# Performance work log

Measured on AMD Instinct MI355X. Metric: run time of the kernel, lower is better.

## Reference

```python
import jax, jax.numpy as jnp
import numpy as np

# 2nd-order Sobel kernels (kornia get_sobel_kernel2d_2nd_order): d2/dx2, d2/dxdy, d2/dy2
_KXX = np.array([[1., -2., 1.], [2., -4., 2.], [1., -2., 1.]], np.float32)
_KXY = np.array([[-1., 0., 1.], [0., 0., 0.], [1., 0., -1.]], np.float32)
_KERNELS = jnp.asarray(np.stack([_KXX, _KXY, _KXX.T])[:, None])  # (3,1,3,3)


def setup_inputs() -> dict:
    key = jax.random.key(0)
    x = jax.random.normal(key, (16, 3, 1024, 1024), dtype=jnp.float32)
    return {"x": x}


def reference(x):
    scale = 1.0
    B, C, H, W = x.shape
    # spatial_gradient_2nd_order: replicate pad + 3x3 conv per channel
    xp = jnp.pad(x.reshape(B * C, 1, H, W), ((0, 0), (0, 0), (1, 1), (1, 1)), mode='edge')
    g = jax.lax.conv_general_dilated(xp, _KERNELS, (1, 1), 'VALID')  # (B*C, 3, H, W)
    gxx, gxy, gyy = g[:, 0], g[:, 1], g[:, 2]
    # abs determinant of Hessian, clamp
    scores = jnp.abs(gxx * gyy - gxy * gxy) * (scale ** 4)
    scores = jnp.maximum(scores, 1e-6).reshape(B, C, H, W)
    # NMS via 3x3 max-pool (stride 1, SAME): keep only local maxima
    pooled = jax.lax.reduce_window(scores, -jnp.inf, jax.lax.max,
                                   (1, 1, 3, 3), (1, 1, 1, 1), 'SAME')
    scores = jnp.where(scores == pooled, scores, jnp.zeros((), scores.dtype))
    # global max normalization (adaptive_max_pool2d to 1x1)
    smax = jnp.max(scores, axis=(2, 3), keepdims=True)  # (B,C,1,1)
    return scores / smax
```

## Files before the change

kernel.cpp:

```cpp
#include <hip/hip_runtime.h>

#define H 1024
#define W 1024
#define HW (H * W)
#define STRIP 16

__device__ __forceinline__ float score_ref(
    float a00, float a01, float a02,
    float a10, float a11, float a12,
    float a20, float a21, float a22)
{
#pragma clang fp contract(off)
    float gxx = fmaf(-2.0f, a01, a00);
    gxx = gxx + a02;
    gxx = fmaf(2.0f, a10, gxx);
    gxx = fmaf(-4.0f, a11, gxx);
    gxx = fmaf(2.0f, a12, gxx);
    gxx = gxx + a20;
    gxx = fmaf(-2.0f, a21, gxx);
    gxx = gxx + a22;
    float gxy = a02 - a00;
    gxy = gxy + a20;
    gxy = gxy - a22;
    float gyy = fmaf(2.0f, a01, a00);
    gyy = gyy + a02;
    gyy = fmaf(-2.0f, a10, gyy);
    gyy = fmaf(-4.0f, a11, gyy);
    gyy = fmaf(-2.0f, a12, gyy);
    gyy = gyy + a20;
    gyy = fmaf(2.0f, a21, gyy);
    gyy = gyy + a22;

    float p1 = gxx * gyy;
    float p2 = gxy * gxy;
    float det = p1 - p2;
    float s = fabsf(det);
    return s > 1e-6f ? s : 1e-6f;
}

struct Row8 { float a[8]; };

__device__ __forceinline__ Row8 load_row8(const float* __restrict__ prow, int c, int t)
{
    const float4 m = *(const float4*)(prow + c);
    int lc = c - 2; lc = lc < 0 ? 0 : lc;
    const float2 L = *(const float2*)(prow + lc);
    int rc = c + 4; rc = rc > (W - 2) ? (W - 2) : rc;
    const float2 R = *(const float2*)(prow + rc);
    float l0 = L.x, l1 = L.y;
    if (t == 0) l1 = L.x;
    float q0 = R.x, q1 = R.y;
    if (t == 255) q0 = R.y;
    Row8 r;
    r.a[0] = l0; r.a[1] = l1;
    r.a[2] = m.x; r.a[3] = m.y; r.a[4] = m.z; r.a[5] = m.w;
    r.a[6] = q0; r.a[7] = q1;
    return r;
}

__global__ __launch_bounds__(256) void hess_max_kernel(
    const float* __restrict__ x, unsigned int* __restrict__ pmax)
{
    const int plane = blockIdx.y;
    const int y0 = blockIdx.x * STRIP;
    const int t = threadIdx.x;
    const int c = t * 4;
    const float* px = x + (size_t)plane * HW;

    Row8 r0 = load_row8(px + (size_t)(y0 - 1 < 0 ? 0 : y0 - 1) * W, c, t);
    Row8 r1 = load_row8(px + (size_t)y0 * W, c, t);
    Row8 r2 = load_row8(px + (size_t)(y0 + 1 > H - 1 ? H - 1 : y0 + 1) * W, c, t);
    Row8 r3 = load_row8(px + (size_t)(y0 + 2 > H - 1 ? H - 1 : y0 + 2) * W, c, t);

    float smax = 1e-6f;
#pragma unroll
    for (int i = 0; i < STRIP; ++i) {
        const int sy = y0 + i;
        const int pf = sy + 3 > H - 1 ? H - 1 : sy + 3;
        Row8 r4 = load_row8(px + (size_t)pf * W, c, t);

        float P[6], Q[6], Rv[6];
#pragma unroll
        for (int k = 0; k < 6; ++k) {
            P[k] = fmaf(2.0f, r1.a[k + 1], r0.a[k + 1]) + r2.a[k + 1];
            Q[k] = fmaf(-2.0f, r1.a[k + 1], r0.a[k + 1]) + r2.a[k + 1];
            Rv[k] = r0.a[k + 1] - r2.a[k + 1];
        }
#pragma unroll
        for (int j = 0; j < 4; ++j) {
            float gxx = fmaf(-2.0f, P[j + 1], P[j]) + P[j + 2];
            float gyy = fmaf(2.0f, Q[j + 1], Q[j]) + Q[j + 2];
            float gxy = Rv[j + 2] - Rv[j];
            float det = fmaf(gxx, gyy, -(gxy * gxy));
            smax = fmaxf(smax, fabsf(det));
        }
        r0 = r1; r1 = r2; r2 = r3; r3 = r4;
    }

#pragma unroll
    for (int off = 32; off > 0; off >>= 1)
        smax = fmaxf(smax, __shfl_down(smax, off));
    if ((t & 63) == 0)
        atomicMax(pmax + plane, __float_as_uint(smax));
}

struct S6 { float s[6]; };

__device__ __forceinline__ S6 score_row_exact(const Row8& A, const Row8& B, const Row8& C)
{
    S6 o;
#pragma unroll
    for (int i = 0; i < 6; ++i)
        o.s[i] = score_ref(A.a[i], A.a[i + 1], A.a[i + 2],
                           B.a[i], B.a[i + 1], B.a[i + 2],
                           C.a[i], C.a[i + 1], C.a[i + 2]);
    return o;
}

__global__ __launch_bounds__(256) void hess_nms_kernel(
    const float* __restrict__ x, const unsigned int* __restrict__ pmax,
    float* __restrict__ out)
{
    const int plane = blockIdx.y;
    const int y0 = blockIdx.x * STRIP;
    const int t = threadIdx.x;
    const int c = t * 4;
    const float* px = x + (size_t)plane * HW;
    float* po = out + (size_t)plane * HW;
    const float inv = 1.0f / __uint_as_float(pmax[plane]);

    Row8 rm2 = load_row8(px + (size_t)(y0 - 2 < 0 ? 0 : y0 - 2) * W, c, t);
    Row8 r0  = load_row8(px + (size_t)(y0 - 1 < 0 ? 0 : y0 - 1) * W, c, t);
    Row8 r1  = load_row8(px + (size_t)y0 * W, c, t);
    Row8 r2  = load_row8(px + (size_t)(y0 + 1 > H - 1 ? H - 1 : y0 + 1) * W, c, t);
    Row8 r3  = load_row8(px + (size_t)(y0 + 2 > H - 1 ? H - 1 : y0 + 2) * W, c, t);

    S6 zero;
#pragma unroll
    for (int i = 0; i < 6; ++i) zero.s[i] = 0.0f;

    S6 sp = zero;
    if (y0 > 0) sp = score_row_exact(rm2, r0, r1);
    S6 sc_ = score_row_exact(r0, r1, r2);

#pragma unroll
    for (int i = 0; i < STRIP; ++i) {
        const int sy = y0 + i;
        const int pf = sy + 3 > H - 1 ? H - 1 : sy + 3;
        Row8 r4 = load_row8(px + (size_t)pf * W, c, t);

        S6 sn = zero;
        if (sy + 1 < H) sn = score_row_exact(r1, r2, r3);

        float4 o;
        float* ov = (float*)&o;
#pragma unroll
        for (int j = 0; j < 4; ++j) {
            float s = sc_.s[j + 1];
            float m = fmaxf(fmaxf(fmaxf(sp.s[j], sp.s[j + 1]), fmaxf(sp.s[j + 2], sc_.s[j])),
                            fmaxf(fmaxf(sc_.s[j + 1], sc_.s[j + 2]),
                                  fmaxf(fmaxf(sn.s[j], sn.s[j + 1]), sn.s[j + 2])));
            ov[j] = (s == m) ? s * inv : 0.0f;
        }
        *(float4*)(po + (size_t)sy * W + c) = o;

        r0 = r1; r1 = r2; r2 = r3; r3 = r4;
        sp = sc_; sc_ = sn;
    }
}

extern "C" void kernel_launch(void* const* d_in, const int* in_sizes, int n_in,
                              void* d_out, int out_size, void* d_ws, size_t ws_size,
                              hipStream_t stream) {
    const float* x = (const float*)d_in[0];
    float* out = (float*)d_out;
    unsigned int* pmax = (unsigned int*)d_ws;
    const int planes = in_sizes[0] / HW;

    hipMemsetAsync(pmax, 0, planes * sizeof(unsigned int), stream);

    dim3 grid(H / STRIP, planes);
    hess_max_kernel<<<grid, 256, 0, stream>>>(x, pmax);
    hess_nms_kernel<<<grid, 256, 0, stream>>>(x, pmax, out);
}
```

Before: 425.3 us.

## Stage input rows through an LDS ring buffer and double strip height

Each thread now issues one float4 global load per row and writes it into a 6-slot LDS ring with replicated edge padding. Neighbour windows are then read back from LDS as two float4s, replacing the overlapping halo float2 global loads. STRIP grows from 16 to 32 so less vertical halo is reloaded per strip. The cost is a __syncthreads per row, LDS traffic, and loops that are no longer unrolled, which may limit memory-level parallelism.

New measurement: 414.6 us. 1.03x faster.

```diff
diff --git a/kernel.cpp b/kernel.cpp
--- a/kernel.cpp
+++ b/kernel.cpp
@@ -3,7 +3,9 @@
 #define H 1024
 #define W 1024
 #define HW (H * W)
-#define STRIP 16
+#define STRIP 32
+#define LDSROW 1032
+#define NSLOT 6
 
 __device__ __forceinline__ float score_ref(
     float a00, float a01, float a02,
@@ -40,51 +42,66 @@
 
 struct Row8 { float a[8]; };
 
-__device__ __forceinline__ Row8 load_row8(const float* __restrict__ prow, int c, int t)
-{
-    const float4 m = *(const float4*)(prow + c);
-    int lc = c - 2; lc = lc < 0 ? 0 : lc;
-    const float2 L = *(const float2*)(prow + lc);
-    int rc = c + 4; rc = rc > (W - 2) ? (W - 2) : rc;
-    const float2 R = *(const float2*)(prow + rc);
-    float l0 = L.x, l1 = L.y;
-    if (t == 0) l1 = L.x;
-    float q0 = R.x, q1 = R.y;
-    if (t == 255) q0 = R.y;
+__device__ __forceinline__ float4 load_row4(const float* __restrict__ px, int row, int t)
+{
+    row = row < 0 ? 0 : (row > H - 1 ? H - 1 : row);
+    return *(const float4*)(px + (size_t)row * W + (t << 2));
+}
+
+__device__ __forceinline__ void stage_row(float* lds, int slot, float4 v, int t)
+{
+    float* p = lds + slot * LDSROW;
+    float* q = p + 2 + (t << 2);
+    *(float2*)(q)     = make_float2(v.x, v.y);
+    *(float2*)(q + 2) = make_float2(v.z, v.w);
+    if (t == 0)   { p[0] = v.x; p[1] = v.x; }
+    if (t == 255) { p[1026] = v.w; p[1027] = v.w; }
+}
+
+__device__ __forceinline__ Row8 read_win(const float* lds, int slot, int t)
+{
+    const float* p = lds + slot * LDSROW + (t << 2);
+    float4 lo = *(const float4*)(p);
+    float4 hi = *(const float4*)(p + 4);
     Row8 r;
-    r.a[0] = l0; r.a[1] = l1;
-    r.a[2] = m.x; r.a[3] = m.y; r.a[4] = m.z; r.a[5] = m.w;
-    r.a[6] = q0; r.a[7] = q1;
+    r.a[0] = lo.x; r.a[1] = lo.y; r.a[2] = lo.z; r.a[3] = lo.w;
+    r.a[4] = hi.x; r.a[5] = hi.y; r.a[6] = hi.z; r.a[7] = hi.w;
     return r;
 }
 
 __global__ __launch_bounds__(256) void hess_max_kernel(
     const float* __restrict__ x, unsigned int* __restrict__ pmax)
 {
+    __shared__ float lds[NSLOT * LDSROW];
     const int plane = blockIdx.y;
     const int y0 = blockIdx.x * STRIP;
     const int t = threadIdx.x;
-    const int c = t * 4;
     const float* px = x + (size_t)plane * HW;
 
-    Row8 r0 = load_row8(px + (size_t)(y0 - 1 < 0 ? 0 : y0 - 1) * W, c, t);
-    Row8 r1 = load_row8(px + (size_t)y0 * W, c, t);
-    Row8 r2 = load_row8(px + (size_t)(y0 + 1 > H - 1 ? H - 1 : y0 + 1) * W, c, t);
-    Row8 r3 = load_row8(px + (size_t)(y0 + 2 > H - 1 ? H - 1 : y0 + 2) * W, c, t);
+    stage_row(lds, 0, load_row4(px, y0 - 1, t), t);
+    stage_row(lds, 1, load_row4(px, y0, t), t);
+    float4 gv = load_row4(px, y0 + 1, t);
+    __syncthreads();
+    Row8 A = read_win(lds, 0, t);
+    Row8 B = read_win(lds, 1, t);
 
     float smax = 1e-6f;
-#pragma unroll
+    int sw = 2;
     for (int i = 0; i < STRIP; ++i) {
         const int sy = y0 + i;
-        const int pf = sy + 3 > H - 1 ? H - 1 : sy + 3;
-        Row8 r4 = load_row8(px + (size_t)pf * W, c, t);
+        stage_row(lds, sw, gv, t);
+        __syncthreads();
+        gv = load_row4(px, sy + 2, t);
+
+        Row8 C = read_win(lds, sw, t);
+        sw = (sw + 1 == NSLOT) ? 0 : sw + 1;
 
         float P[6], Q[6], Rv[6];
 #pragma unroll
         for (int k = 0; k < 6; ++k) {
-            P[k] = fmaf(2.0f, r1.a[k + 1], r0.a[k + 1]) + r2.a[k + 1];
-            Q[k] = fmaf(-2.0f, r1.a[k + 1], r0.a[k + 1]) + r2.a[k + 1];
-            Rv[k] = r0.a[k + 1] - r2.a[k + 1];
+            P[k]  = fmaf(2.0f, B.a[k + 1], A.a[k + 1]) + C.a[k + 1];
+            Q[k]  = fmaf(-2.0f, B.a[k + 1], A.a[k + 1]) + C.a[k + 1];
+            Rv[k] = A.a[k + 1] - C.a[k + 1];
         }
 #pragma unroll
         for (int j = 0; j < 4; ++j) {
@@ -94,7 +111,7 @@
             float det = fmaf(gxx, gyy, -(gxy * gxy));
             smax = fmaxf(smax, fabsf(det));
         }
-        r0 = r1; r1 = r2; r2 = r3; r3 = r4;
+        A = B; B = C;
     }
 
 #pragma unroll
@@ -121,19 +138,26 @@
     const float* __restrict__ x, const unsigned int* __restrict__ pmax,
     float* __restrict__ out)
 {
+    __shared__ float lds[NSLOT * LDSROW];
     const int plane = blockIdx.y;
     const int y0 = blockIdx.x * STRIP;
     const int t = threadIdx.x;
-    const int c = t * 4;
     const float* px = x + (size_t)plane * HW;
     float* po = out + (size_t)plane * HW;
     const float inv = 1.0f / __uint_as_float(pmax[plane]);
 
-    Row8 rm2 = load_row8(px + (size_t)(y0 - 2 < 0 ? 0 : y0 - 2) * W, c, t);
-    Row8 r0  = load_row8(px + (size_t)(y0 - 1 < 0 ? 0 : y0 - 1) * W, c, t);
-    Row8 r1  = load_row8(px + (size_t)y0 * W, c, t);
-    Row8 r2  = load_row8(px + (size_t)(y0 + 1 > H - 1 ? H - 1 : y0 + 1) * W, c, t);
-    Row8 r3  = load_row8(px + (size_t)(y0 + 2 > H - 1 ? H - 1 : y0 + 2) * W, c, t);
+    stage_row(lds, 0, load_row4(px, y0 - 2, t), t);
+    stage_row(lds, 1, load_row4(px, y0 - 1, t), t);
+    stage_row(lds, 2, load_row4(px, y0,     t), t);
+    stage_row(lds, 3, load_row4(px, y0 + 1, t), t);
+    stage_row(lds, 4, load_row4(px, y0 + 2, t), t);
+    float4 gv = load_row4(px, y0 + 3, t);
+    __syncthreads();
+    Row8 rm2 = read_win(lds, 0, t);
+    Row8 r0  = read_win(lds, 1, t);
+    Row8 r1  = read_win(lds, 2, t);
+    Row8 r2  = read_win(lds, 3, t);
+    Row8 r3  = read_win(lds, 4, t);
 
     S6 zero;
 #pragma unroll
@@ -143,11 +167,12 @@
     if (y0 > 0) sp = score_row_exact(rm2, r0, r1);
     S6 sc_ = score_row_exact(r0, r1, r2);
 
-#pragma unroll
+    int sw = 5;
     for (int i = 0; i < STRIP; ++i) {
         const int sy = y0 + i;
-        const int pf = sy + 3 > H - 1 ? H - 1 : sy + 3;
-        Row8 r4 = load_row8(px + (size_t)pf * W, c, t);
+        stage_row(lds, sw, gv, t);
+        __syncthreads();
+        gv = load_row4(px, sy + 4, t);
 
         S6 sn = zero;
         if (sy + 1 < H) sn = score_row_exact(r1, r2, r3);
@@ -162,9 +187,11 @@
                                   fmaxf(fmaxf(sn.s[j], sn.s[j + 1]), sn.s[j + 2])));
             ov[j] = (s == m) ? s * inv : 0.0f;
         }
-        *(float4*)(po + (size_t)sy * W + c) = o;
-
-        r0 = r1; r1 = r2; r2 = r3; r3 = r4;
+        *(float4*)(po + (size_t)sy * W + (t << 2)) = o;
+
+        Row8 r4 = read_win(lds, sw, t);
+        sw = (sw + 1 == NSLOT) ? 0 : sw + 1;
+        r1 = r2; r2 = r3; r3 = r4;
         sp = sc_; sc_ = sn;
     }
 }
```

## Stage input rows through an LDS ring via async global_load_lds and double strip height

Applied to the files above, without the earlier changes.

Both kernels now stream input rows into a six-slot LDS ring using the direct global-to-LDS load builtin, with vmcnt waits plus barriers pipelining the prefetch, instead of each thread issuing three overlapping global loads per row. The strip height doubles to 32 rows, which cuts the redundant halo-row reads between blocks, and the output uses nontemporal stores. This removes duplicated global traffic for the neighbour columns and gives explicit prefetch depth. In exchange it adds per-row block barriers, LDS use that can lower occupancy, and fragile hand-counted waitcnt logic.

Result: faster. 411.7 us (-3.2%).

```diff
diff --git a/kernel.cpp b/kernel.cpp
--- a/kernel.cpp
+++ b/kernel.cpp
@@ -3,7 +3,30 @@
 #define H 1024
 #define W 1024
 #define HW (H * W)
-#define STRIP 16
+#define STRIP 32
+#define SLOTF 1024
+#define RING 6
+
+typedef __attribute__((address_space(3))) float lds_f;
+typedef const __attribute__((address_space(1))) float g_f;
+typedef float nfloat4 __attribute__((ext_vector_type(4)));
+
+__device__ __forceinline__ void gload16(const float* g, float* l) {
+    __builtin_amdgcn_global_load_lds((g_f*)g, (lds_f*)l, 16, 0, 0);
+}
+
+template<int N>
+__device__ __forceinline__ void wait_vm_barrier() {
+    asm volatile("s_waitcnt vmcnt(%0)\n\ts_barrier" :: "i"(N) : "memory");
+}
+__device__ __forceinline__ void barrier_only() {
+    asm volatile("s_barrier" ::: "memory");
+}
+
+__device__ __forceinline__ void stage(const float* px, int row, float* slotbase, int wq, int t) {
+    row = row < 0 ? 0 : (row > H - 1 ? H - 1 : row);
+    gload16(px + (size_t)row * W + (t << 2), slotbase + wq);
+}
 
 __device__ __forceinline__ float score_ref(
     float a00, float a01, float a02,
@@ -40,51 +63,57 @@
 
 struct Row8 { float a[8]; };
 
-__device__ __forceinline__ Row8 load_row8(const float* __restrict__ prow, int c, int t)
-{
-    const float4 m = *(const float4*)(prow + c);
-    int lc = c - 2; lc = lc < 0 ? 0 : lc;
-    const float2 L = *(const float2*)(prow + lc);
-    int rc = c + 4; rc = rc > (W - 2) ? (W - 2) : rc;
-    const float2 R = *(const float2*)(prow + rc);
-    float l0 = L.x, l1 = L.y;
-    if (t == 0) l1 = L.x;
-    float q0 = R.x, q1 = R.y;
-    if (t == 255) q0 = R.y;
+__device__ __forceinline__ Row8 read_win(const float* p, int t)
+{
+    const int c = t << 2;
+    const float2 L  = *(const float2*)(p + (t == 0 ? 0 : c - 2));
+    const float4 M  = *(const float4*)(p + c);
+    const float2 Rr = *(const float2*)(p + (t == 255 ? 1022 : c + 4));
     Row8 r;
-    r.a[0] = l0; r.a[1] = l1;
-    r.a[2] = m.x; r.a[3] = m.y; r.a[4] = m.z; r.a[5] = m.w;
-    r.a[6] = q0; r.a[7] = q1;
+    r.a[0] = L.x;
+    r.a[1] = (t == 0) ? L.x : L.y;
+    r.a[2] = M.x; r.a[3] = M.y; r.a[4] = M.z; r.a[5] = M.w;
+    r.a[6] = (t == 255) ? Rr.y : Rr.x;
+    r.a[7] = Rr.y;
     return r;
 }
 
 __global__ __launch_bounds__(256) void hess_max_kernel(
     const float* __restrict__ x, unsigned int* __restrict__ pmax)
 {
+    __shared__ float lds[RING * SLOTF];
     const int plane = blockIdx.y;
     const int y0 = blockIdx.x * STRIP;
     const int t = threadIdx.x;
-    const int c = t * 4;
+    const int wq = (t >> 6) << 8;
     const float* px = x + (size_t)plane * HW;
 
-    Row8 r0 = load_row8(px + (size_t)(y0 - 1 < 0 ? 0 : y0 - 1) * W, c, t);
-    Row8 r1 = load_row8(px + (size_t)y0 * W, c, t);
-    Row8 r2 = load_row8(px + (size_t)(y0 + 1 > H - 1 ? H - 1 : y0 + 1) * W, c, t);
-    Row8 r3 = load_row8(px + (size_t)(y0 + 2 > H - 1 ? H - 1 : y0 + 2) * W, c, t);
+#pragma unroll
+    for (int k = 0; k < RING; ++k)
+        stage(px, y0 - 1 + k, lds + k * SLOTF, wq, t);
+    wait_vm_barrier<4>();
+    Row8 A = read_win(lds, t);
+    Row8 B = read_win(lds + SLOTF, t);
 
     float smax = 1e-6f;
-#pragma unroll
+    int si = 0, sr = 2;
     for (int i = 0; i < STRIP; ++i) {
-        const int sy = y0 + i;
-        const int pf = sy + 3 > H - 1 ? H - 1 : sy + 3;
-        Row8 r4 = load_row8(px + (size_t)pf * W, c, t);
+        if (i < STRIP - 4) {
+            stage(px, y0 + i + 5, lds + si * SLOTF, wq, t);
+            si = si + 1 == RING ? 0 : si + 1;
+            wait_vm_barrier<4>();
+        } else {
+            wait_vm_barrier<0>();
+        }
+        Row8 C = read_win(lds + sr * SLOTF, t);
+        sr = sr + 1 == RING ? 0 : sr + 1;
 
         float P[6], Q[6], Rv[6];
 #pragma unroll
         for (int k = 0; k < 6; ++k) {
-            P[k] = fmaf(2.0f, r1.a[k + 1], r0.a[k + 1]) + r2.a[k + 1];
-            Q[k] = fmaf(-2.0f, r1.a[k + 1], r0.a[k + 1]) + r2.a[k + 1];
-            Rv[k] = r0.a[k + 1] - r2.a[k + 1];
+            P[k]  = fmaf(2.0f, B.a[k + 1], A.a[k + 1]) + C.a[k + 1];
+            Q[k]  = fmaf(-2.0f, B.a[k + 1], A.a[k + 1]) + C.a[k + 1];
+            Rv[k] = A.a[k + 1] - C.a[k + 1];
         }
 #pragma unroll
         for (int j = 0; j < 4; ++j) {
@@ -94,7 +123,7 @@
             float det = fmaf(gxx, gyy, -(gxy * gxy));
             smax = fmaxf(smax, fabsf(det));
         }
-        r0 = r1; r1 = r2; r2 = r3; r3 = r4;
+        A = B; B = C;
     }
 
 #pragma unroll
@@ -121,19 +150,24 @@
     const float* __restrict__ x, const unsigned int* __restrict__ pmax,
     float* __restrict__ out)
 {
+    __shared__ float lds[RING * SLOTF];
     const int plane = blockIdx.y;
     const int y0 = blockIdx.x * STRIP;
     const int t = threadIdx.x;
-    const int c = t * 4;
+    const int wq = (t >> 6) << 8;
     const float* px = x + (size_t)plane * HW;
     float* po = out + (size_t)plane * HW;
     const float inv = 1.0f / __uint_as_float(pmax[plane]);
 
-    Row8 rm2 = load_row8(px + (size_t)(y0 - 2 < 0 ? 0 : y0 - 2) * W, c, t);
-    Row8 r0  = load_row8(px + (size_t)(y0 - 1 < 0 ? 0 : y0 - 1) * W, c, t);
-    Row8 r1  = load_row8(px + (size_t)y0 * W, c, t);
-    Row8 r2  = load_row8(px + (size_t)(y0 + 1 > H - 1 ? H - 1 : y0 + 1) * W, c, t);
-    Row8 r3  = load_row8(px + (size_t)(y0 + 2 > H - 1 ? H - 1 : y0 + 2) * W, c, t);
+#pragma unroll
+    for (int k = 0; k < RING; ++k)
+        stage(px, y0 - 2 + k, lds + k * SLOTF, wq, t);
+    wait_vm_barrier<1>();
+    Row8 rm2 = read_win(lds, t);
+    Row8 r0  = read_win(lds + SLOTF, t);
+    Row8 r1  = read_win(lds + 2 * SLOTF, t);
+    Row8 r2  = read_win(lds + 3 * SLOTF, t);
+    Row8 r3  = read_win(lds + 4 * SLOTF, t);
 
     S6 zero;
 #pragma unroll
@@ -143,28 +177,41 @@
     if (y0 > 0) sp = score_row_exact(rm2, r0, r1);
     S6 sc_ = score_row_exact(r0, r1, r2);
 
-#pragma unroll
+    barrier_only();
+    stage(px, y0 + 4, lds + 0 * SLOTF, wq, t);
+    stage(px, y0 + 5, lds + 1 * SLOTF, wq, t);
+
+    int si = 2, sr = 5;
     for (int i = 0; i < STRIP; ++i) {
         const int sy = y0 + i;
-        const int pf = sy + 3 > H - 1 ? H - 1 : sy + 3;
-        Row8 r4 = load_row8(px + (size_t)pf * W, c, t);
+        if (i < STRIP - 3) {
+            stage(px, y0 + i + 6, lds + si * SLOTF, wq, t);
+            si = si + 1 == RING ? 0 : si + 1;
+        }
+        if (i == 0)               wait_vm_barrier<3>();
+        else if (i == 1)          wait_vm_barrier<4>();
+        else if (i == 2)          wait_vm_barrier<5>();
+        else if (i < STRIP - 3)   wait_vm_barrier<6>();
+        else                      wait_vm_barrier<0>();
+
+        Row8 r4 = read_win(lds + sr * SLOTF, t);
+        sr = sr + 1 == RING ? 0 : sr + 1;
 
         S6 sn = zero;
         if (sy + 1 < H) sn = score_row_exact(r1, r2, r3);
 
-        float4 o;
-        float* ov = (float*)&o;
+        nfloat4 o;
 #pragma unroll
         for (int j = 0; j < 4; ++j) {
             float s = sc_.s[j + 1];
             float m = fmaxf(fmaxf(fmaxf(sp.s[j], sp.s[j + 1]), fmaxf(sp.s[j + 2], sc_.s[j])),
                             fmaxf(fmaxf(sc_.s[j + 1], sc_.s[j + 2]),
                                   fmaxf(fmaxf(sn.s[j], sn.s[j + 1]), sn.s[j + 2])));
-            ov[j] = (s == m) ? s * inv : 0.0f;
-        }
-        *(float4*)(po + (size_t)sy * W + c) = o;
-
-        r0 = r1; r1 = r2; r2 = r3; r3 = r4;
+            o[j] = (s == m) ? s * inv : 0.0f;
+        }
+        __builtin_nontemporal_store(o, (nfloat4*)(po + (size_t)sy * W + (t << 2)));
+
+        r1 = r2; r2 = r3; r3 = r4;
         sp = sc_; sc_ = sn;
     }
 }
```
